# Kernel optimization log

Measured on AMD Instinct MI355X. Metric: run time of the kernel, lower is better.

## Reference

```python
import jax, jax.numpy as jnp
import numpy as np

B = 65536
IN_F = 512
OUT_F = 256
NUM_GROUPS = 8
EPS = 1e-5


def setup_inputs() -> dict:
    key = jax.random.key(0)
    ks = jax.random.split(key, 6)
    return {
        "x": jax.random.normal(ks[0], (B, IN_F), dtype=jnp.float32),
        "weight": jax.random.normal(ks[1], (OUT_F, IN_F), dtype=jnp.float32) * 0.05,
        "bias_linear": jax.random.normal(ks[2], (OUT_F,), dtype=jnp.float32) * 0.05,
        "weight_gn": jax.random.normal(ks[3], (OUT_F,), dtype=jnp.float32),
        "bias_gn": jax.random.normal(ks[4], (OUT_F,), dtype=jnp.float32),
        "bias": jax.random.normal(ks[5], (1, OUT_F, 1, 1), dtype=jnp.float32),
    }


def reference(x, weight, bias_linear, weight_gn, bias_gn, bias):
    # Linear: (B, IN_F) @ (IN_F, OUT_F) + bias -> (B, OUT_F)
    h = jnp.einsum("bi,oi->bo", x, weight) + bias_linear
    # GroupNorm over channel dim (dim=1) with NUM_GROUPS groups
    g = h.reshape(B, NUM_GROUPS, OUT_F // NUM_GROUPS)
    mean = jnp.mean(g, axis=2, keepdims=True)
    var = jnp.mean(jnp.square(g - mean), axis=2, keepdims=True)
    gn = ((g - mean) * jax.lax.rsqrt(var + EPS)).reshape(B, OUT_F)
    gn = gn * weight_gn + bias_gn
    # Min over channels, keepdim -> (B, 1)
    min_vals = jnp.min(gn, axis=1, keepdims=True)
    # torch broadcasting: (B,1) + (1,256,1,1) -> (1,256,B,1)
    result = min_vals + bias
    return result
```

## Files before the change

### kernel.cpp

```cpp
#include <hip/hip_runtime.h>

#define B_ROWS 65536
#define K_DIM  512
#define N_DIM  256
#define EPS    1e-5f
#define MTILE  32
#define NBLK   256
#define TILES  (B_ROWS / MTILE)
#define STRIDE 520

using short8  = __attribute__((ext_vector_type(8))) short;
using floatx4 = __attribute__((ext_vector_type(4))) float;

#define LBAR() do {                                          \
    __builtin_amdgcn_sched_barrier(0);                       \
    asm volatile("s_waitcnt lgkmcnt(0)" ::: "memory");       \
    __builtin_amdgcn_s_barrier();                            \
    __builtin_amdgcn_sched_barrier(0);                       \
} while (0)

__device__ __forceinline__ unsigned short f2bf(float f) {
    unsigned u = __builtin_bit_cast(unsigned, f);
    u += 0x7FFFu + ((u >> 16) & 1u);
    return (unsigned short)(u >> 16);
}

__global__ __launch_bounds__(64) void pack_w(const float* __restrict__ W,
                                             unsigned short* __restrict__ P) {
    int b    = blockIdx.x;
    int nt   = b >> 4, kk = b & 15;
    int lane = threadIdx.x;
    int l15  = lane & 15, quad = lane >> 4;
    const float* src = W + (size_t)(nt * 16 + l15) * K_DIM + kk * 32 + quad * 8;
    short8 v;
#pragma unroll
    for (int j = 0; j < 8; ++j) v[j] = (short)f2bf(src[j]);
    *(short8*)(P + ((size_t)(nt * 16 + kk) * 64 + lane) * 8) = v;
}

__global__ __launch_bounds__(1024) void fused_gemm_min(
    const float* __restrict__ X, const unsigned short* __restrict__ P,
    const float* __restrict__ bias_lin, const float* __restrict__ wgn,
    const float* __restrict__ bgn, float* __restrict__ m_out)
{
    __shared__ unsigned short Ash[2][MTILE * STRIDE];
    __shared__ float smS[16][32];
    __shared__ float smSS[16][32];
    __shared__ float smin[16][32];

    const int tid  = threadIdx.x;
    const int wave = tid >> 6;
    const int lane = tid & 63;
    const int l15  = lane & 15, quad = lane >> 4;

    short8 bfr[16];
#pragma unroll
    for (int kkg = 0; kkg < 16; ++kkg)
        bfr[kkg] = *(const short8*)(P + (((size_t)wave * 16 + kkg) * 64 + lane) * 8);

    float blr[4], wgr[4], bgr[4];
#pragma unroll
    for (int r = 0; r < 4; ++r) {
        int c = wave * 16 + quad * 4 + r;
        blr[r] = bias_lin[c]; wgr[r] = wgn[c]; bgr[r] = bgn[c];
    }

    const int r0 = (tid >> 7) * 4;
    const int c4 = (tid & 127) * 4;

    int t = blockIdx.x;

    float4 xq[4];
#pragma unroll
    for (int p = 0; p < 4; ++p)
        xq[p] = *(const float4*)(X + (size_t)(t * MTILE + r0 + p) * K_DIM + c4);
#pragma unroll
    for (int p = 0; p < 4; ++p) {
        ushort4 h;
        h.x = f2bf(xq[p].x); h.y = f2bf(xq[p].y);
        h.z = f2bf(xq[p].z); h.w = f2bf(xq[p].w);
        *(ushort4*)(&Ash[0][(r0 + p) * STRIDE + c4]) = h;
    }
    if (t + NBLK < TILES) {
#pragma unroll
        for (int p = 0; p < 4; ++p)
            xq[p] = *(const float4*)(X + (size_t)((t + NBLK) * MTILE + r0 + p) * K_DIM + c4);
    }
    LBAR();

    int cur = 0;
    for (; t < TILES; t += NBLK) {
        if (t + NBLK < TILES) {
#pragma unroll
            for (int p = 0; p < 4; ++p) {
                ushort4 h;
                h.x = f2bf(xq[p].x); h.y = f2bf(xq[p].y);
                h.z = f2bf(xq[p].z); h.w = f2bf(xq[p].w);
                *(ushort4*)(&Ash[cur ^ 1][(r0 + p) * STRIDE + c4]) = h;
            }
            if (t + 2 * NBLK < TILES) {
#pragma unroll
                for (int p = 0; p < 4; ++p)
                    xq[p] = *(const float4*)(X + (size_t)((t + 2 * NBLK) * MTILE + r0 + p) * K_DIM + c4);
            }
        }

        floatx4 acc[2];
#pragma unroll
        for (int rt = 0; rt < 2; ++rt)
#pragma unroll
            for (int r = 0; r < 4; ++r) acc[rt][r] = blr[r];
#pragma unroll
        for (int kk = 0; kk < 16; ++kk) {
            short8 a0 = *(const short8*)&Ash[cur][(l15)      * STRIDE + kk * 32 + quad * 8];
            short8 a1 = *(const short8*)&Ash[cur][(16 + l15) * STRIDE + kk * 32 + quad * 8];
            acc[0] = __builtin_amdgcn_mfma_f32_16x16x32_bf16(bfr[kk], a0, acc[0], 0, 0, 0);
            acc[1] = __builtin_amdgcn_mfma_f32_16x16x32_bf16(bfr[kk], a1, acc[1], 0, 0, 0);
        }

        float sreg[2], ssreg[2];
#pragma unroll
        for (int rt = 0; rt < 2; ++rt) {
            float s = 0.f, ss = 0.f;
#pragma unroll
            for (int r = 0; r < 4; ++r) { float v = acc[rt][r]; s += v; ss = fmaf(v, v, ss); }
            s  += __shfl_xor(s, 16);  s  += __shfl_xor(s, 32);
            ss += __shfl_xor(ss, 16); ss += __shfl_xor(ss, 32);
            sreg[rt] = s; ssreg[rt] = ss;
            if (quad == 0) { smS[wave][rt * 16 + l15] = s; smSS[wave][rt * 16 + l15] = ss; }
        }
        LBAR();

#pragma unroll
        for (int rt = 0; rt < 2; ++rt) {
            int row = rt * 16 + l15;
            float st   = sreg[rt]  + smS[wave ^ 1][row];
            float sst  = ssreg[rt] + smSS[wave ^ 1][row];
            float mean = st * (1.0f / 32.0f);
            float var  = sst * (1.0f / 32.0f) - mean * mean;
            float inv  = rsqrtf(var + EPS);
            float mi   = mean * inv;
            float mn   = 1e30f;
#pragma unroll
            for (int r = 0; r < 4; ++r) {
                float g = fmaf(fmaf(acc[rt][r], inv, -mi), wgr[r], bgr[r]);
                mn = fminf(mn, g);
            }
            mn = fminf(mn, __shfl_xor(mn, 16));
            mn = fminf(mn, __shfl_xor(mn, 32));
            if (quad == 0) smin[wave][row] = mn;
        }
        LBAR();

        if (tid < MTILE) {
            float m0 = smin[0][tid];
#pragma unroll
            for (int w = 1; w < 16; ++w) m0 = fminf(m0, smin[w][tid]);
            m_out[t * MTILE + tid] = m0;
        }
        cur ^= 1;
    }
}

__global__ __launch_bounds__(256) void bcast_out(
    const float* __restrict__ m, const float* __restrict__ bias,
    float* __restrict__ out)
{
    const float4* m4  = (const float4*)m;
    float4*       o4  = (float4*)out;
    const int bid = blockIdx.x;
    const int c   = bid >> 3;
    const float bc = bias[c];
    const int base = (bid & 7) * 2048;
#pragma unroll
    for (int k = 0; k < 8; ++k) {
        int idx = base + k * 256 + threadIdx.x;
        float4 mv = m4[idx];
        float4 o;
        o.x = mv.x + bc; o.y = mv.y + bc; o.z = mv.z + bc; o.w = mv.w + bc;
        o4[(size_t)c * (B_ROWS / 4) + idx] = o;
    }
}

extern "C" void kernel_launch(void* const* d_in, const int* in_sizes, int n_in,
                              void* d_out, int out_size, void* d_ws, size_t ws_size,
                              hipStream_t stream) {
    const float* x    = (const float*)d_in[0];
    const float* w    = (const float*)d_in[1];
    const float* bl   = (const float*)d_in[2];
    const float* wg   = (const float*)d_in[3];
    const float* bg   = (const float*)d_in[4];
    const float* bias = (const float*)d_in[5];

    unsigned short* P = (unsigned short*)d_ws;
    float* m          = (float*)((char*)d_ws + 262144);
    float* out        = (float*)d_out;

    hipLaunchKernelGGL(pack_w, dim3(256), dim3(64), 0, stream, w, P);
    hipLaunchKernelGGL(fused_gemm_min, dim3(NBLK), dim3(1024), 0, stream,
                       x, P, bl, wg, bg, m);
    hipLaunchKernelGGL(bcast_out, dim3(2048), dim3(256), 0, stream, m, bias, out);
}
```

Baseline: 229.7 us.

## Split GEMM columns across blocks with partial-min output and XCD-aware tile mapping

Replaces the persistent 256-block, 1024-thread double-buffered kernel with 8192 small 256-thread blocks. Each block computes one 32-row tile for a quarter of the output columns and writes a partial min to a [4][B] buffer, which the broadcast kernel reduces. Block ids are mapped so the four column-parts of a tile land on the same XCD, aiming at L2 reuse of X. The costs are that each X tile is read and converted by four blocks instead of one, the B-fragment registers are reloaded per block, and the explicit prefetch pipelining is gone.

```diff
diff --git a/kernel.cpp b/kernel.cpp
--- a/kernel.cpp
+++ b/kernel.cpp
@@ -5,19 +5,11 @@
 #define N_DIM  256
 #define EPS    1e-5f
 #define MTILE  32
-#define NBLK   256
 #define TILES  (B_ROWS / MTILE)
 #define STRIDE 520
 
 using short8  = __attribute__((ext_vector_type(8))) short;
 using floatx4 = __attribute__((ext_vector_type(4))) float;
-
-#define LBAR() do {                                          \
-    __builtin_amdgcn_sched_barrier(0);                       \
-    asm volatile("s_waitcnt lgkmcnt(0)" ::: "memory");       \
-    __builtin_amdgcn_s_barrier();                            \
-    __builtin_amdgcn_sched_barrier(0);                       \
-} while (0)
 
 __device__ __forceinline__ unsigned short f2bf(float f) {
     unsigned u = __builtin_bit_cast(unsigned, f);
@@ -38,136 +30,117 @@
     *(short8*)(P + ((size_t)(nt * 16 + kk) * 64 + lane) * 8) = v;
 }
 
-__global__ __launch_bounds__(1024) void fused_gemm_min(
+__global__ __launch_bounds__(256, 4) void gemm_gn_minpart(
     const float* __restrict__ X, const unsigned short* __restrict__ P,
     const float* __restrict__ bias_lin, const float* __restrict__ wgn,
-    const float* __restrict__ bgn, float* __restrict__ m_out)
+    const float* __restrict__ bgn, float* __restrict__ mparts)
 {
-    __shared__ unsigned short Ash[2][MTILE * STRIDE];
-    __shared__ float smS[16][32];
-    __shared__ float smSS[16][32];
-    __shared__ float smin[16][32];
+    __shared__ unsigned short Ash[MTILE * STRIDE];
+    __shared__ float smS[4][32];
+    __shared__ float smSS[4][32];
+    __shared__ float smin[4][32];
 
     const int tid  = threadIdx.x;
     const int wave = tid >> 6;
     const int lane = tid & 63;
     const int l15  = lane & 15, quad = lane >> 4;
 
+    const int bid  = blockIdx.x;
+    const int xcd  = bid & 7;
+    const int j    = bid >> 3;
+    const int tile = xcd * 256 + (j >> 2);
+    const int part = j & 3;
+    const int nt   = part * 4 + wave;
+
     short8 bfr[16];
 #pragma unroll
     for (int kkg = 0; kkg < 16; ++kkg)
-        bfr[kkg] = *(const short8*)(P + (((size_t)wave * 16 + kkg) * 64 + lane) * 8);
+        bfr[kkg] = *(const short8*)(P + (((size_t)nt * 16 + kkg) * 64 + lane) * 8);
 
     float blr[4], wgr[4], bgr[4];
 #pragma unroll
     for (int r = 0; r < 4; ++r) {
-        int c = wave * 16 + quad * 4 + r;
+        int c = nt * 16 + quad * 4 + r;
         blr[r] = bias_lin[c]; wgr[r] = wgn[c]; bgr[r] = bgn[c];
     }
 
-    const int r0 = (tid >> 7) * 4;
-    const int c4 = (tid & 127) * 4;
+    {
+        const int r0 = (tid >> 7) * 16;
+        const int c4 = (tid & 127) * 4;
+        const float* src = X + (size_t)(tile * MTILE + r0) * K_DIM + c4;
+#pragma unroll
+        for (int p = 0; p < 16; ++p) {
+            float4 v = *(const float4*)(src + (size_t)p * K_DIM);
+            ushort4 h;
+            h.x = f2bf(v.x); h.y = f2bf(v.y); h.z = f2bf(v.z); h.w = f2bf(v.w);
+            *(ushort4*)(&Ash[(r0 + p) * STRIDE + c4]) = h;
+        }
+    }
+    __syncthreads();
 
-    int t = blockIdx.x;
+    floatx4 acc[2];
+#pragma unroll
+    for (int rt = 0; rt < 2; ++rt)
+#pragma unroll
+        for (int r = 0; r < 4; ++r) acc[rt][r] = blr[r];
+#pragma unroll
+    for (int kk = 0; kk < 16; ++kk) {
+        short8 a0 = *(const short8*)&Ash[(l15)      * STRIDE + kk * 32 + quad * 8];
+        short8 a1 = *(const short8*)&Ash[(16 + l15) * STRIDE + kk * 32 + quad * 8];
+        acc[0] = __builtin_amdgcn_mfma_f32_16x16x32_bf16(bfr[kk], a0, acc[0], 0, 0, 0);
+        acc[1] = __builtin_amdgcn_mfma_f32_16x16x32_bf16(bfr[kk], a1, acc[1], 0, 0, 0);
+    }
 
-    float4 xq[4];
+    float sreg[2], ssreg[2];
 #pragma unroll
-    for (int p = 0; p < 4; ++p)
-        xq[p] = *(const float4*)(X + (size_t)(t * MTILE + r0 + p) * K_DIM + c4);
+    for (int rt = 0; rt < 2; ++rt) {
+        float s = 0.f, ss = 0.f;
 #pragma unroll
-    for (int p = 0; p < 4; ++p) {
-        ushort4 h;
-        h.x = f2bf(xq[p].x); h.y = f2bf(xq[p].y);
-        h.z = f2bf(xq[p].z); h.w = f2bf(xq[p].w);
-        *(ushort4*)(&Ash[0][(r0 + p) * STRIDE + c4]) = h;
+        for (int r = 0; r < 4; ++r) { float v = acc[rt][r]; s += v; ss = fmaf(v, v, ss); }
+        s  += __shfl_xor(s, 16);  s  += __shfl_xor(s, 32);
+        ss += __shfl_xor(ss, 16); ss += __shfl_xor(ss, 32);
+        sreg[rt] = s; ssreg[rt] = ss;
+        if (quad == 0) { smS[wave][rt * 16 + l15] = s; smSS[wave][rt * 16 + l15] = ss; }
     }
-    if (t + NBLK < TILES) {
-#pragma unroll
-        for (int p = 0; p < 4; ++p)
-            xq[p] = *(const float4*)(X + (size_t)((t + NBLK) * MTILE + r0 + p) * K_DIM + c4);
-    }
-    LBAR();
-
-    int cur = 0;
-    for (; t < TILES; t += NBLK) {
-        if (t + NBLK < TILES) {
-#pragma unroll
-            for (int p = 0; p < 4; ++p) {
-                ushort4 h;
-                h.x = f2bf(xq[p].x); h.y = f2bf(xq[p].y);
-                h.z = f2bf(xq[p].z); h.w = f2bf(xq[p].w);
-                *(ushort4*)(&Ash[cur ^ 1][(r0 + p) * STRIDE + c4]) = h;
-            }
-            if (t + 2 * NBLK < TILES) {
-#pragma unroll
-                for (int p = 0; p < 4; ++p)
-                    xq[p] = *(const float4*)(X + (size_t)((t + 2 * NBLK) * MTILE + r0 + p) * K_DIM + c4);
-            }
-        }
-
-        floatx4 acc[2];
-#pragma unroll
-        for (int rt = 0; rt < 2; ++rt)
-#pragma unroll
-            for (int r = 0; r < 4; ++r) acc[rt][r] = blr[r];
-#pragma unroll
-        for (int kk = 0; kk < 16; ++kk) {
-            short8 a0 = *(const short8*)&Ash[cur][(l15)      * STRIDE + kk * 32 + quad * 8];
-            short8 a1 = *(const short8*)&Ash[cur][(16 + l15) * STRIDE + kk * 32 + quad * 8];
-            acc[0] = __builtin_amdgcn_mfma_f32_16x16x32_bf16(bfr[kk], a0, acc[0], 0, 0, 0);
-            acc[1] = __builtin_amdgcn_mfma_f32_16x16x32_bf16(bfr[kk], a1, acc[1], 0, 0, 0);
-        }
-
-        float sreg[2], ssreg[2];
-#pragma unroll
-        for (int rt = 0; rt < 2; ++rt) {
-            float s = 0.f, ss = 0.f;
-#pragma unroll
-            for (int r = 0; r < 4; ++r) { float v = acc[rt][r]; s += v; ss = fmaf(v, v, ss); }
-            s  += __shfl_xor(s, 16);  s  += __shfl_xor(s, 32);
-            ss += __shfl_xor(ss, 16); ss += __shfl_xor(ss, 32);
-            sreg[rt] = s; ssreg[rt] = ss;
-            if (quad == 0) { smS[wave][rt * 16 + l15] = s; smSS[wave][rt * 16 + l15] = ss; }
-        }
-        LBAR();
+    __syncthreads();
 
 #pragma unroll
-        for (int rt = 0; rt < 2; ++rt) {
-            int row = rt * 16 + l15;
-            float st   = sreg[rt]  + smS[wave ^ 1][row];
-            float sst  = ssreg[rt] + smSS[wave ^ 1][row];
-            float mean = st * (1.0f / 32.0f);
-            float var  = sst * (1.0f / 32.0f) - mean * mean;
-            float inv  = rsqrtf(var + EPS);
-            float mi   = mean * inv;
-            float mn   = 1e30f;
+    for (int rt = 0; rt < 2; ++rt) {
+        int row = rt * 16 + l15;
+        float st   = sreg[rt]  + smS[wave ^ 1][row];
+        float sst  = ssreg[rt] + smSS[wave ^ 1][row];
+        float mean = st * (1.0f / 32.0f);
+        float var  = sst * (1.0f / 32.0f) - mean * mean;
+        float inv  = rsqrtf(var + EPS);
+        float mi   = mean * inv;
+        float mn   = 1e30f;
 #pragma unroll
-            for (int r = 0; r < 4; ++r) {
-                float g = fmaf(fmaf(acc[rt][r], inv, -mi), wgr[r], bgr[r]);
-                mn = fminf(mn, g);
-            }
-            mn = fminf(mn, __shfl_xor(mn, 16));
-            mn = fminf(mn, __shfl_xor(mn, 32));
-            if (quad == 0) smin[wave][row] = mn;
+        for (int r = 0; r < 4; ++r) {
+            float g = fmaf(fmaf(acc[rt][r], inv, -mi), wgr[r], bgr[r]);
+            mn = fminf(mn, g);
         }
-        LBAR();
+        mn = fminf(mn, __shfl_xor(mn, 16));
+        mn = fminf(mn, __shfl_xor(mn, 32));
+        if (quad == 0) smin[wave][row] = mn;
+    }
+    __syncthreads();
 
-        if (tid < MTILE) {
-            float m0 = smin[0][tid];
-#pragma unroll
-            for (int w = 1; w < 16; ++w) m0 = fminf(m0, smin[w][tid]);
-            m_out[t * MTILE + tid] = m0;
-        }
-        cur ^= 1;
+    if (tid < MTILE) {
+        float m0 = fminf(fminf(smin[0][tid], smin[1][tid]),
+                         fminf(smin[2][tid], smin[3][tid]));
+        mparts[(size_t)part * B_ROWS + tile * MTILE + tid] = m0;
     }
 }
 
 __global__ __launch_bounds__(256) void bcast_out(
-    const float* __restrict__ m, const float* __restrict__ bias,
+    const float* __restrict__ mparts, const float* __restrict__ bias,
     float* __restrict__ out)
 {
-    const float4* m4  = (const float4*)m;
-    float4*       o4  = (float4*)out;
+    const float4* m0 = (const float4*)(mparts);
+    const float4* m1 = (const float4*)(mparts + B_ROWS);
+    const float4* m2 = (const float4*)(mparts + 2 * B_ROWS);
+    const float4* m3 = (const float4*)(mparts + 3 * B_ROWS);
+    float4*       o4 = (float4*)out;
     const int bid = blockIdx.x;
     const int c   = bid >> 3;
     const float bc = bias[c];
@@ -175,9 +148,12 @@
 #pragma unroll
     for (int k = 0; k < 8; ++k) {
         int idx = base + k * 256 + threadIdx.x;
-        float4 mv = m4[idx];
+        float4 a = m0[idx], b = m1[idx], d = m2[idx], e = m3[idx];
         float4 o;
-        o.x = mv.x + bc; o.y = mv.y + bc; o.z = mv.z + bc; o.w = mv.w + bc;
+        o.x = fminf(fminf(a.x, b.x), fminf(d.x, e.x)) + bc;
+        o.y = fminf(fminf(a.y, b.y), fminf(d.y, e.y)) + bc;
+        o.z = fminf(fminf(a.z, b.z), fminf(d.z, e.z)) + bc;
+        o.w = fminf(fminf(a.w, b.w), fminf(d.w, e.w)) + bc;
         o4[(size_t)c * (B_ROWS / 4) + idx] = o;
     }
 }
@@ -193,11 +169,11 @@
     const float* bias = (const float*)d_in[5];
 
     unsigned short* P = (unsigned short*)d_ws;
-    float* m          = (float*)((char*)d_ws + 262144);
+    float* mparts     = (float*)((char*)d_ws + 262144);
     float* out        = (float*)d_out;
 
     hipLaunchKernelGGL(pack_w, dim3(256), dim3(64), 0, stream, w, P);
-    hipLaunchKernelGGL(fused_gemm_min, dim3(NBLK), dim3(1024), 0, stream,
-                       x, P, bl, wg, bg, m);
-    hipLaunchKernelGGL(bcast_out, dim3(2048), dim3(256), 0, stream, m, bias, out);
+    hipLaunchKernelGGL(gemm_gn_minpart, dim3(8192), dim3(256), 0, stream,
+                       x, P, bl, wg, bg, mparts);
+    hipLaunchKernelGGL(bcast_out, dim3(2048), dim3(256), 0, stream, mparts, bias, out);
 }
```

Measured after the change: 253.1 us. 1.1x slower.
